# Performance work log

Measured on AMD Instinct MI355X. Metric: run time of the kernel, lower is better.

The kernel has to match this reference:

```python
import jax, jax.numpy as jnp
import numpy as np

D_H, HEAD, LAYER_IDX = 1024, 16, 11
D_ATTN = D_H // HEAD
BZ, LEN = 2, 2048


def setup_inputs() -> dict:
    key = jax.random.key(0)
    ks = jax.random.split(key, 8)
    s = 1.0 / np.sqrt(D_H)
    v = jax.random.normal(ks[0], (BZ, LEN, D_H), jnp.float32)
    k = jax.random.normal(ks[1], (BZ, LEN, D_H), jnp.float32)
    q = jax.random.normal(ks[2], (BZ, LEN, D_H), jnp.float32)
    # causal mask: 1.0 where attention is blocked (j > i)
    causal = jnp.triu(jnp.ones((LEN, LEN), jnp.float32), k=1)
    mask = jnp.broadcast_to(causal[None, None], (BZ, 1, LEN, LEN))
    Wv = jax.random.normal(ks[3], (D_H, D_H), jnp.float32) * s
    Wk = jax.random.normal(ks[4], (D_H, D_H), jnp.float32) * s
    Wq = jax.random.normal(ks[5], (D_H, D_H), jnp.float32) * s
    Wo = jax.random.normal(ks[6], (D_H, D_H), jnp.float32) * s
    bo = jnp.zeros((D_H,), jnp.float32)
    return {"v": v, "k": k, "q": q, "mask": mask,
            "Wv": Wv, "Wk": Wk, "Wq": Wq, "Wo": Wo, "bo": bo}


def _split_head(x):
    # (bz, len, d_h) -> (bz, head, len, d_attn)
    bz, L, _ = x.shape
    return x.reshape(bz, L, HEAD, D_ATTN).transpose(0, 2, 1, 3)


def reference(v, k, q, mask, Wv, Wk, Wq, Wo, bo):
    bz, len_q, _ = q.shape
    vh = _split_head(v @ Wv)  # (bz, head, len_k, d_attn)
    kh = _split_head(k @ Wk)
    qh = _split_head(q @ Wq)
    scale = 1.0 / jnp.sqrt(jnp.asarray(D_ATTN, jnp.float32))
    weight = jnp.einsum("bhqd,bhkd->bhqk", qh, kh) * scale
    weight = weight + mask * (-1e9)
    weight = weight / jnp.asarray(LAYER_IDX + 1, jnp.float32)
    attn = jax.nn.softmax(weight, axis=-1)  # dropout omitted (inference)
    out = jnp.einsum("bhqk,bhkd->bhqd", attn, vh)
    out = out.transpose(0, 2, 1, 3).reshape(bz, len_q, D_H)
    return out @ Wo + bo
```

## Files before the change

### kernel.cpp

```cpp
#include <hip/hip_runtime.h>
#include <hip/hip_fp16.h>

typedef _Float16 f16;
typedef _Float16 f16x4 __attribute__((ext_vector_type(4)));
typedef _Float16 f16x8 __attribute__((ext_vector_type(8)));
typedef float f32x4 __attribute__((ext_vector_type(4)));
typedef float f32x16 __attribute__((ext_vector_type(16)));

#define D_H   1024
#define LEN   2048
#define BZ    2
#define NHEAD 16
#define DA    64
#define MTOK  (BZ * LEN)
#define KDIM  1024
#define ATT_SCALE (0.125f / 12.0f)

__device__ __forceinline__ void load_lds16(const f16* g, f16* l) {
  __builtin_amdgcn_global_load_lds((const __attribute__((address_space(1))) void*)g,
                                   (__attribute__((address_space(3))) void*)l,
                                   16, 0, 0);
}

#define FENCE() __asm__ volatile("" ::: "memory")

__device__ __forceinline__ unsigned pk2(float a, float b) {
  union { f16 h; unsigned short u; } ca, cb;
  ca.h = (f16)a; cb.h = (f16)b;
  return (unsigned)ca.u | ((unsigned)cb.u << 16);
}

__global__ __launch_bounds__(256)
void k_prep(const float* __restrict__ W0, const float* __restrict__ W1,
            const float* __restrict__ W2, const float* __restrict__ W3,
            const float* __restrict__ xq, const float* __restrict__ xk,
            const float* __restrict__ xv,
            f16* __restrict__ T0, f16* __restrict__ T1,
            f16* __restrict__ T2, f16* __restrict__ T3,
            f16* __restrict__ q16, f16* __restrict__ k16,
            f16* __restrict__ v16) {
  const int z = blockIdx.z;
  const int tid = threadIdx.x;
  if (z < 4) {
    const float* W = (z == 0) ? W0 : (z == 1) ? W1 : (z == 2) ? W2 : W3;
    f16* Wt = (z == 0) ? T0 : (z == 1) ? T1 : (z == 2) ? T2 : T3;
    __shared__ float tile[64][68];
    const int r0 = blockIdx.y * 64, c0 = blockIdx.x * 64;
    {
      const int row = tid >> 2, cq = (tid & 3) * 16;
      const float* src = W + (size_t)(r0 + row) * D_H + c0 + cq;
      float4 v0 = *(const float4*)(src + 0);
      float4 v1 = *(const float4*)(src + 4);
      float4 v2 = *(const float4*)(src + 8);
      float4 v3 = *(const float4*)(src + 12);
      *(float4*)&tile[row][cq + 0]  = v0;
      *(float4*)&tile[row][cq + 4]  = v1;
      *(float4*)&tile[row][cq + 8]  = v2;
      *(float4*)&tile[row][cq + 12] = v3;
    }
    __syncthreads();
    {
      const int c = tid >> 2, rq = (tid & 3) * 16;
      f16 ov[16];
#pragma unroll
      for (int j = 0; j < 16; ++j) ov[j] = (f16)tile[rq + j][c];
      f16* dst = Wt + (size_t)(c0 + c) * D_H + r0 + rq;
      *(f16x8*)(dst + 0) = *(f16x8*)&ov[0];
      *(f16x8*)(dst + 8) = *(f16x8*)&ov[8];
    }
  } else {
    const float* in = (z == 4) ? xq : (z == 5) ? xk : xv;
    f16* out = (z == 4) ? q16 : (z == 5) ? k16 : v16;
    const size_t blk = ((size_t)(blockIdx.y * 16 + blockIdx.x)) * 16384;
#pragma unroll
    for (int s = 0; s < 16; ++s) {
      size_t off = blk + (size_t)(s * 256 + tid) * 4;
      float4 x = *(const float4*)(in + off);
      f16x4 o; o[0] = (f16)x.x; o[1] = (f16)x.y; o[2] = (f16)x.z; o[3] = (f16)x.w;
      *(f16x4*)(out + off) = o;
    }
  }
}

#define BM2 256
#define BN2 256
#define BKT 64
#define NKT (KDIM / BKT)

__global__ __launch_bounds__(512, 2)
void k_gemm3(const f16* __restrict__ A0, const f16* __restrict__ A1,
             const f16* __restrict__ A2, const f16* __restrict__ W0,
             const f16* __restrict__ W1, const f16* __restrict__ W2,
             f16* __restrict__ O0, f16* __restrict__ O1, f16* __restrict__ O2) {
  __shared__ __align__(16) f16 smem3[65536];
  f16* As = smem3;
  f16* Bs = smem3 + 32768;
  const int lin = blockIdx.x + 16 * blockIdx.y + 64 * blockIdx.z;
  const int w = (lin & 7) * 24 + (lin >> 3);
  const int z = w >> 6;
  const int rem = w & 63;
  const int m0 = (rem >> 2) * BM2, n0 = (rem & 3) * BN2;
  const f16* A = (z == 0) ? A0 : (z == 1) ? A1 : A2;
  const f16* Bt = (z == 0) ? W0 : (z == 1) ? W1 : W2;
  f16* Out = (z == 0) ? O0 : (z == 1) ? O1 : O2;
  const int tid = threadIdx.x;
  const int wave = tid >> 6, lane = tid & 63;
  const int lc = lane & 15, quad = lane >> 4;
  const int wr = wave >> 2, wc = wave & 3;
  const f16* Ab = A + (size_t)m0 * KDIM;
  const f16* Bb = Bt + (size_t)n0 * KDIM;

  f32x4 acc[8][4] = {};

#define STAGE_HALF(g, ldsbase, kt, h)                                         \
  {                                                                           \
    _Pragma("unroll")                                                         \
    for (int r = 0; r < 2; ++r) {                                             \
      int idx = tid + r * 512;                                                \
      int row = (h) * 128 + (idx >> 3);                                       \
      int gch = (idx & 7) ^ (row & 7);                                        \
      load_lds16((g) + (size_t)row * KDIM + (kt) * BKT + gch * 8,             \
                 (ldsbase) + (h) * 8192 + idx * 8);                           \
    }                                                                         \
  }

#define READ_A(mh, kc)                                                        \
  _Pragma("unroll")                                                           \
  for (int i = 0; i < 4; ++i) {                                               \
    int row = wr * 128 + ((mh) * 4 + i) * 16 + lc;                            \
    int pc = ((kc) * 4 + quad) ^ (row & 7);                                   \
    af[i] = *(const f16x8*)&Ad[row * 64 + pc * 8];                            \
  }
#define READ_B(kc)                                                            \
  _Pragma("unroll")                                                           \
  for (int n = 0; n < 4; ++n) {                                               \
    int row = wc * 64 + n * 16 + lc;                                          \
    int pc = ((kc) * 4 + quad) ^ (row & 7);                                   \
    bf[n] = *(const f16x8*)&Bd[row * 64 + pc * 8];                            \
  }
#define MFMA_Q(mh)                                                            \
  FENCE(); __builtin_amdgcn_s_barrier();                                      \
  __builtin_amdgcn_s_setprio(1);                                              \
  _Pragma("unroll")                                                           \
  for (int i = 0; i < 4; ++i)                                                 \
    _Pragma("unroll")                                                         \
    for (int n = 0; n < 4; ++n)                                               \
      acc[(mh) * 4 + i][n] = __builtin_amdgcn_mfma_f32_16x16x32_f16(          \
          af[i], bf[n], acc[(mh) * 4 + i][n], 0, 0, 0);                       \
  __builtin_amdgcn_s_setprio(0);                                              \
  __asm__ volatile("s_waitcnt lgkmcnt(0)" ::: "memory");                      \
  FENCE(); __builtin_amdgcn_s_barrier(); FENCE();

  STAGE_HALF(Ab, As, 0, 0);
  STAGE_HALF(Ab, As, 0, 1);
  STAGE_HALF(Bb, Bs, 0, 0);
  STAGE_HALF(Bb, Bs, 0, 1);
  STAGE_HALF(Ab, As + 16384, 1, 0);
  __asm__ volatile("s_waitcnt vmcnt(2)" ::: "memory");
  __builtin_amdgcn_s_barrier();
  FENCE();

  for (int t = 0; t < NKT; ++t) {
    const f16* Ad = As + (t & 1) * 16384;
    const f16* Bd = Bs + (t & 1) * 16384;
    f16* AdW = As + (t & 1) * 16384;
    f16* Adn = As + ((t + 1) & 1) * 16384;
    f16* Bdn = Bs + ((t + 1) & 1) * 16384;
    const bool pf = (t + 1 < NKT);
    f16x8 af[4], bf[4];

    READ_A(0, 0); READ_B(0);
    if (pf) STAGE_HALF(Ab, Adn, t + 1, 1);
    MFMA_Q(0);

    READ_A(1, 0);
    if (pf) STAGE_HALF(Bb, Bdn, t + 1, 0);
    MFMA_Q(1);

    READ_A(0, 1); READ_B(1);
    if (pf) STAGE_HALF(Bb, Bdn, t + 1, 1);
    MFMA_Q(0);

    READ_A(1, 1);
    FENCE(); __builtin_amdgcn_s_barrier();
    if (t + 2 < NKT) STAGE_HALF(Ab, AdW, t + 2, 0);
    __builtin_amdgcn_s_setprio(1);
#pragma unroll
    for (int i = 0; i < 4; ++i)
#pragma unroll
      for (int n = 0; n < 4; ++n)
        acc[4 + i][n] = __builtin_amdgcn_mfma_f32_16x16x32_f16(
            af[i], bf[n], acc[4 + i][n], 0, 0, 0);
    __builtin_amdgcn_s_setprio(0);
    if (t + 2 < NKT) {
      __asm__ volatile("s_waitcnt vmcnt(2)" ::: "memory");
    } else if (pf) {
      __asm__ volatile("s_waitcnt vmcnt(0)" ::: "memory");
    }
    __asm__ volatile("s_waitcnt lgkmcnt(0)" ::: "memory");
    FENCE(); __builtin_amdgcn_s_barrier(); FENCE();
  }

  if (z <= 1) {
    f16* slice = smem3 + wave * 8192;
#pragma unroll
    for (int mi = 0; mi < 8; ++mi)
#pragma unroll
      for (int ni = 0; ni < 4; ++ni)
#pragma unroll
        for (int rr = 0; rr < 4; ++rr) {
          int tl = mi * 16 + quad * 4 + rr;
          int d = ni * 16 + lc;
          slice[tl * 64 + (((d >> 3) ^ (tl & 7)) << 3) + (d & 7)] =
              (f16)acc[mi][ni][rr];
        }
    __asm__ volatile("s_waitcnt lgkmcnt(0)" ::: "memory");
    const int h = (n0 >> 6) + wc;
    const int tokbase = m0 + wr * 128;
    const int b = tokbase >> 11, ib = tokbase & 2047;
#pragma unroll
    for (int s = 0; s < 16; ++s) {
      int u = lane + s * 64;
      int tl = u >> 3, ch = u & 7;
      f16x8 vv = *(const f16x8*)&slice[tl * 64 + ((ch ^ (tl & 7)) << 3)];
      *(f16x8*)(Out + ((size_t)((b << 4) + h) * LEN + ib + tl) * DA + ch * 8) = vv;
    }
  } else {
    f16* Ct = smem3;
#pragma unroll
    for (int e = 0; e < 2; ++e) {
      __syncthreads();
      if (wr == e) {
#pragma unroll
        for (int mi = 0; mi < 8; ++mi)
#pragma unroll
          for (int ni = 0; ni < 4; ++ni)
#pragma unroll
            for (int rr = 0; rr < 4; ++rr) {
              int tl = mi * 16 + quad * 4 + rr;
              int dl = wc * 64 + ni * 16 + lc;
              Ct[dl * 136 + tl] = (f16)acc[mi][ni][rr];
            }
      }
      __syncthreads();
      const int tokbase = m0 + e * 128;
      const int b = tokbase >> 11, j0 = tokbase & 2047;
#pragma unroll
      for (int s = 0; s < 8; ++s) {
        int u = tid + s * 512;
        int dl = u >> 4, ch = u & 15;
        f16x8 vv = *(const f16x8*)&Ct[dl * 136 + ch * 8];
        *(f16x8*)(Out + ((size_t)(b * 1024 + n0 + dl)) * LEN + j0 + ch * 8) = vv;
      }
    }
  }
}

#define OM 64
#define ON 128
#define BK 64
#define ONIT (KDIM / BK)
__global__ __launch_bounds__(256)
void k_gemm_out(const f16* __restrict__ A, const f16* __restrict__ Bt,
                float* __restrict__ Out, const float* __restrict__ bias) {
  __shared__ __align__(16) char smem[2 * (OM + ON) * BK * 2];
  f16* As = (f16*)smem;
  f16* Bs = As + 2 * OM * BK;
  const int m0 = blockIdx.x * OM, n0 = blockIdx.y * ON;
  const int tid = threadIdx.x;
  const int wave = tid >> 6, lane = tid & 63;
  const int lc = lane & 15, quad = lane >> 4;
  const int wm = (wave >> 1) * 32, wn = (wave & 1) * 64;
  const int swz = lc & 7;
  const f16* Abase = A + (size_t)m0 * KDIM;
  const f16* Bbase = Bt + (size_t)n0 * KDIM;

  f32x4 acc[2][4] = {};

#define STAGE_OUT(t)                                                          \
  {                                                                           \
    int k0s = (t) * BK;                                                       \
    f16* Ad = As + ((t) & 1) * (OM * BK);                                     \
    f16* Bd = Bs + ((t) & 1) * (ON * BK);                                     \
    _Pragma("unroll")                                                         \
    for (int r = 0; r < 2; ++r) {                                             \
      int idx = tid + r * 256;                                                \
      int row = idx >> 3, ch = idx & 7;                                       \
      int gch = ch ^ (row & 7);                                               \
      load_lds16(Abase + (size_t)row * KDIM + k0s + gch * 8, &Ad[idx * 8]);   \
    }                                                                         \
    _Pragma("unroll")                                                         \
    for (int r = 0; r < 4; ++r) {                                             \
      int idx = tid + r * 256;                                                \
      int row = idx >> 3, ch = idx & 7;                                       \
      int gch = ch ^ (row & 7);                                               \
      load_lds16(Bbase + (size_t)row * KDIM + k0s + gch * 8, &Bd[idx * 8]);   \
    }                                                                         \
  }

  STAGE_OUT(0);
  for (int t = 0; t < ONIT; ++t) {
    __syncthreads();
    if (t + 1 < ONIT) STAGE_OUT(t + 1);
    const f16* Ad = As + (t & 1) * (OM * BK);
    const f16* Bd = Bs + (t & 1) * (ON * BK);
    __builtin_amdgcn_s_setprio(1);
#pragma unroll
    for (int kc = 0; kc < 2; ++kc) {
      f16x8 af[2], bf[4];
#pragma unroll
      for (int mi = 0; mi < 2; ++mi)
        af[mi] = *(const f16x8*)&Ad[(wm + mi * 16 + lc) * 64 +
                                    (((kc * 4 + quad) ^ swz) * 8)];
#pragma unroll
      for (int ni = 0; ni < 4; ++ni)
        bf[ni] = *(const f16x8*)&Bd[(wn + ni * 16 + lc) * 64 +
                                    (((kc * 4 + quad) ^ swz) * 8)];
#pragma unroll
      for (int mi = 0; mi < 2; ++mi)
#pragma unroll
        for (int ni = 0; ni < 4; ++ni)
          acc[mi][ni] = __builtin_amdgcn_mfma_f32_16x16x32_f16(
              af[mi], bf[ni], acc[mi][ni], 0, 0, 0);
    }
    __builtin_amdgcn_s_setprio(0);
  }

  float* Ct = (float*)smem;
#pragma unroll
  for (int hf = 0; hf < 2; ++hf) {
    __syncthreads();
    if ((wave & 1) == hf) {
#pragma unroll
      for (int mi = 0; mi < 2; ++mi)
#pragma unroll
        for (int ni = 0; ni < 4; ++ni)
#pragma unroll
          for (int r = 0; r < 4; ++r) {
            int tok = wm + mi * 16 + quad * 4 + r;
            int d = ni * 16 + lc;
            Ct[tok * 68 + d] = acc[mi][ni][r];
          }
    }
    __syncthreads();
#pragma unroll
    for (int it = 0; it < 4; ++it) {
      int u = tid + it * 256;
      int tok = u >> 4, ch = u & 15;
      int gm = m0 + tok;
      int gc = n0 + hf * 64 + ch * 4;
      float4 bv = *(const float4*)(bias + gc);
      float4 cv = *(const float4*)&Ct[tok * 68 + ch * 4];
      float4 ov;
      ov.x = cv.x + bv.x; ov.y = cv.y + bv.y;
      ov.z = cv.z + bv.z; ov.w = cv.w + bv.w;
      *(float4*)(Out + (size_t)gm * D_H + gc) = ov;
    }
  }
}

__global__ __launch_bounds__(256, 2)
void k_attn(const f16* __restrict__ Qh, const f16* __restrict__ Kh,
            const f16* __restrict__ Vt, f16* __restrict__ O16) {
  const int tid = threadIdx.x;
  const int wid = blockIdx.x * 4 + (tid >> 6);
  const int lane = tid & 63;
  const int cq = lane & 31, half = lane >> 5;
  const int jb = (wid < 1024) ? (63 - (wid >> 5)) : ((wid - 1024) >> 5);
  const int bh = wid & 31;
  const int b = bh >> 4, h = bh & 15;
  const f16* Qb = Qh + (size_t)bh * LEN * DA;
  const f16* Kb = Kh + (size_t)bh * LEN * DA;
  const f16* Vb = Vt + (size_t)bh * DA * LEN;
  const f16 qs = (f16)(ATT_SCALE * 1.44269504088896340736f);

  f16x8 qf[4];
#pragma unroll
  for (int d = 0; d < 4; ++d) {
    qf[d] = *(const f16x8*)(Qb + (size_t)(jb * 32 + cq) * DA + d * 16 + half * 8);
#pragma unroll
    for (int j = 0; j < 8; ++j) qf[d][j] = qf[d][j] * qs;
  }

  f32x16 acc0 = {}, acc1 = {};
  float lsum = 0.f;

#define AT_LOAD(tt, KF, VF)                                                   \
  {                                                                           \
    const f16* kp = Kb + (size_t)((tt) * 32 + cq) * DA + half * 8;            \
    KF[0] = *(const f16x8*)(kp);                                              \
    KF[1] = *(const f16x8*)(kp + 16);                                         \
    KF[2] = *(const f16x8*)(kp + 32);                                         \
    KF[3] = *(const f16x8*)(kp + 48);                                         \
    const f16* vp0 = Vb + (size_t)cq * LEN + (tt) * 32 + half * 8;            \
    const f16* vp1 = Vb + (size_t)(32 + cq) * LEN + (tt) * 32 + half * 8;     \
    VF[0] = *(const f16x8*)(vp0);                                             \
    VF[1] = *(const f16x8*)(vp1);                                             \
    VF[2] = *(const f16x8*)(vp0 + 16);                                        \
    VF[3] = *(const f16x8*)(vp1 + 16);                                        \
  }

#define AT_COMPUTE(tt, KF, VF)                                                \
  {                                                                           \
    f32x16 st = {};                                                           \
    st = __builtin_amdgcn_mfma_f32_32x32x16_f16(KF[0], qf[0], st, 0, 0, 0);   \
    st = __builtin_amdgcn_mfma_f32_32x32x16_f16(KF[1], qf[1], st, 0, 0, 0);   \
    st = __builtin_amdgcn_mfma_f32_32x32x16_f16(KF[2], qf[2], st, 0, 0, 0);   \
    st = __builtin_amdgcn_mfma_f32_32x32x16_f16(KF[3], qf[3], st, 0, 0, 0);   \
    float ev[16];                                                             \
    if ((tt) == jb) {                                                         \
      _Pragma("unroll")                                                       \
      for (int r = 0; r < 16; ++r) {                                          \
        int kl = (r & 3) + 8 * (r >> 2) + 4 * half;                           \
        float e = exp2f(st[r]);                                               \
        ev[r] = (kl > cq) ? 0.f : e;                                          \
      }                                                                       \
    } else {                                                                  \
      _Pragma("unroll")                                                       \
      for (int r = 0; r < 16; ++r) ev[r] = exp2f(st[r]);                      \
    }                                                                         \
    lsum += (((ev[0] + ev[1]) + (ev[2] + ev[3])) +                            \
             ((ev[4] + ev[5]) + (ev[6] + ev[7]))) +                           \
            (((ev[8] + ev[9]) + (ev[10] + ev[11])) +                          \
             ((ev[12] + ev[13]) + (ev[14] + ev[15])));                        \
    unsigned w0 = pk2(ev[0], ev[1]),  w1 = pk2(ev[2], ev[3]);                 \
    unsigned w2 = pk2(ev[4], ev[5]),  w3 = pk2(ev[6], ev[7]);                 \
    unsigned w4 = pk2(ev[8], ev[9]),  w5 = pk2(ev[10], ev[11]);               \
    unsigned w6 = pk2(ev[12], ev[13]), w7 = pk2(ev[14], ev[15]);              \
    unsigned p0 = __shfl_xor((int)w0, 32, 64), p1 = __shfl_xor((int)w1, 32, 64);\
    unsigned p2 = __shfl_xor((int)w2, 32, 64), p3 = __shfl_xor((int)w3, 32, 64);\
    unsigned p4 = __shfl_xor((int)w4, 32, 64), p5 = __shfl_xor((int)w5, 32, 64);\
    unsigned p6 = __shfl_xor((int)w6, 32, 64), p7 = __shfl_xor((int)w7, 32, 64);\
    union { unsigned u[4]; f16x8 v; } A0, A1;                                 \
    A0.u[0] = half ? p2 : w0;  A0.u[1] = half ? p3 : w1;                      \
    A0.u[2] = half ? w2 : p0;  A0.u[3] = half ? w3 : p1;                      \
    A1.u[0] = half ? p6 : w4;  A1.u[1] = half ? p7 : w5;                      \
    A1.u[2] = half ? w6 : p4;  A1.u[3] = half ? w7 : p5;                      \
    acc0 = __builtin_amdgcn_mfma_f32_32x32x16_f16(A0.v, VF[0], acc0, 0, 0, 0);\
    acc1 = __builtin_amdgcn_mfma_f32_32x32x16_f16(A0.v, VF[1], acc1, 0, 0, 0);\
    acc0 = __builtin_amdgcn_mfma_f32_32x32x16_f16(A1.v, VF[2], acc0, 0, 0, 0);\
    acc1 = __builtin_amdgcn_mfma_f32_32x32x16_f16(A1.v, VF[3], acc1, 0, 0, 0);\
  }

  f16x8 kfA[4], vfA[4], kfB[4], vfB[4];
  const int niter = jb + 1;
  AT_LOAD(0, kfA, vfA);
  int t = 0;
  for (; t + 1 < niter; t += 2) {
    AT_LOAD(t + 1, kfB, vfB);
    AT_COMPUTE(t, kfA, vfA);
    if (t + 2 < niter) AT_LOAD(t + 2, kfA, vfA);
    AT_COMPUTE(t + 1, kfB, vfB);
  }
  if (t < niter) AT_COMPUTE(t, kfA, vfA);

  lsum += __shfl_xor(lsum, 32, 64);
  const size_t obase = ((size_t)b * LEN + jb * 32) * D_H + h * DA;
#pragma unroll
  for (int r = 0; r < 16; ++r) {
    int rq = (r & 3) + 8 * (r >> 2) + 4 * half;
    float ls = __shfl(lsum, rq, 64);
    float inv = 1.0f / ls;
    O16[obase + (size_t)rq * D_H + cq] = (f16)(acc0[r] * inv);
    O16[obase + (size_t)rq * D_H + 32 + cq] = (f16)(acc1[r] * inv);
  }
}

extern "C" void kernel_launch(void* const* d_in, const int* in_sizes, int n_in,
                              void* d_out, int out_size, void* d_ws, size_t ws_size,
                              hipStream_t stream) {
  const float* v_f = (const float*)d_in[0];
  const float* k_f = (const float*)d_in[1];
  const float* q_f = (const float*)d_in[2];
  const float* Wv = (const float*)d_in[4];
  const float* Wk = (const float*)d_in[5];
  const float* Wq = (const float*)d_in[6];
  const float* Wo = (const float*)d_in[7];
  const float* bo = (const float*)d_in[8];
  float* out = (float*)d_out;

  const size_t SZ_X = (size_t)MTOK * D_H;
  const size_t SZ_W = (size_t)D_H * D_H;
  f16* ws = (f16*)d_ws;
  f16* q16 = ws;
  f16* k16 = ws + SZ_X;
  f16* v16 = ws + 2 * SZ_X;
  f16* Qh  = ws + 3 * SZ_X;
  f16* Kh  = ws + 4 * SZ_X;
  f16* Vt  = ws + 5 * SZ_X;
  f16* Wqt = ws + 6 * SZ_X;
  f16* Wkt = Wqt + SZ_W;
  f16* Wvt = Wqt + 2 * SZ_W;
  f16* Wot = Wqt + 3 * SZ_W;
  f16* O16 = q16;

  k_prep<<<dim3(16, 16, 7), 256, 0, stream>>>(
      Wq, Wk, Wv, Wo, q_f, k_f, v_f, Wqt, Wkt, Wvt, Wot, q16, k16, v16);

  k_gemm3<<<dim3(MTOK / BM2, D_H / BN2, 3), 512, 0, stream>>>(
      q16, k16, v16, Wqt, Wkt, Wvt, Qh, Kh, Vt);

  k_attn<<<dim3(512), 256, 0, stream>>>(Qh, Kh, Vt, O16);

  k_gemm_out<<<dim3(MTOK / OM, D_H / ON), 256, 0, stream>>>(O16, Wot, out, bo);
}
```

Measured before the change: 244.0 us.

## Split attention key range across wave pairs and combine partials via LDS

Each query tile is now processed by two waves that each cover half of the causal key tiles. The second wave writes its partial accumulators and row sums to shared memory, and the first wave adds them and writes the normalized output. The grid doubles and launch bounds rise to 4 blocks per CU. The aim is to shorten the critical path of long causal rows and raise occupancy, at the cost of a block-wide sync, an LDS reduction and register pressure under the tighter bound.

Result: slower. 336.5 us (+37.9%).

```diff
diff --git a/kernel.cpp b/kernel.cpp
--- a/kernel.cpp
+++ b/kernel.cpp
@@ -359,20 +359,27 @@
   }
 }
 
-__global__ __launch_bounds__(256, 2)
+__global__ __launch_bounds__(256, 4)
 void k_attn(const f16* __restrict__ Qh, const f16* __restrict__ Kh,
             const f16* __restrict__ Vt, f16* __restrict__ O16) {
+  __shared__ float comb[2][64][33];
   const int tid = threadIdx.x;
-  const int wid = blockIdx.x * 4 + (tid >> 6);
-  const int lane = tid & 63;
+  const int wave = tid >> 6, lane = tid & 63;
   const int cq = lane & 31, half = lane >> 5;
-  const int jb = (wid < 1024) ? (63 - (wid >> 5)) : ((wid - 1024) >> 5);
-  const int bh = wid & 31;
+  const int pairId = wave >> 1, ks = wave & 1;
+  const int bh = blockIdx.x & 31;
+  const int p = blockIdx.x >> 5;
+  const int jb = pairId ? p : 63 - p;
   const int b = bh >> 4, h = bh & 15;
   const f16* Qb = Qh + (size_t)bh * LEN * DA;
   const f16* Kb = Kh + (size_t)bh * LEN * DA;
   const f16* Vb = Vt + (size_t)bh * DA * LEN;
   const f16 qs = (f16)(ATT_SCALE * 1.44269504088896340736f);
+
+  const int nT = jb + 1;
+  const int nA = (nT + 1) >> 1;
+  const int t0 = ks ? nA : 0;
+  const int cnt = ks ? (nT - nA) : nA;
 
   f16x8 qf[4];
 #pragma unroll
@@ -442,27 +449,46 @@
     acc1 = __builtin_amdgcn_mfma_f32_32x32x16_f16(A1.v, VF[3], acc1, 0, 0, 0);\
   }
 
-  f16x8 kfA[4], vfA[4], kfB[4], vfB[4];
-  const int niter = jb + 1;
-  AT_LOAD(0, kfA, vfA);
-  int t = 0;
-  for (; t + 1 < niter; t += 2) {
-    AT_LOAD(t + 1, kfB, vfB);
-    AT_COMPUTE(t, kfA, vfA);
-    if (t + 2 < niter) AT_LOAD(t + 2, kfA, vfA);
-    AT_COMPUTE(t + 1, kfB, vfB);
-  }
-  if (t < niter) AT_COMPUTE(t, kfA, vfA);
-
-  lsum += __shfl_xor(lsum, 32, 64);
-  const size_t obase = ((size_t)b * LEN + jb * 32) * D_H + h * DA;
-#pragma unroll
-  for (int r = 0; r < 16; ++r) {
-    int rq = (r & 3) + 8 * (r >> 2) + 4 * half;
-    float ls = __shfl(lsum, rq, 64);
-    float inv = 1.0f / ls;
-    O16[obase + (size_t)rq * D_H + cq] = (f16)(acc0[r] * inv);
-    O16[obase + (size_t)rq * D_H + 32 + cq] = (f16)(acc1[r] * inv);
+  if (cnt > 0) {
+    f16x8 kfA[4], vfA[4], kfB[4], vfB[4];
+    const int tend = t0 + cnt;
+    AT_LOAD(t0, kfA, vfA);
+    int t = t0;
+    for (; t + 1 < tend; t += 2) {
+      AT_LOAD(t + 1, kfB, vfB);
+      AT_COMPUTE(t, kfA, vfA);
+      if (t + 2 < tend) AT_LOAD(t + 2, kfA, vfA);
+      AT_COMPUTE(t + 1, kfB, vfB);
+    }
+    if (t < tend) AT_COMPUTE(t, kfA, vfA);
+  }
+
+  if (ks == 1) {
+#pragma unroll
+    for (int r = 0; r < 16; ++r) {
+      comb[pairId][lane][r] = acc0[r];
+      comb[pairId][lane][16 + r] = acc1[r];
+    }
+    comb[pairId][lane][32] = lsum;
+  }
+  __syncthreads();
+  if (ks == 0) {
+#pragma unroll
+    for (int r = 0; r < 16; ++r) {
+      acc0[r] += comb[pairId][lane][r];
+      acc1[r] += comb[pairId][lane][16 + r];
+    }
+    lsum += comb[pairId][lane][32];
+    lsum += __shfl_xor(lsum, 32, 64);
+    const size_t obase = ((size_t)b * LEN + jb * 32) * D_H + h * DA;
+#pragma unroll
+    for (int r = 0; r < 16; ++r) {
+      int rq = (r & 3) + 8 * (r >> 2) + 4 * half;
+      float ls = __shfl(lsum, rq, 64);
+      float inv = 1.0f / ls;
+      O16[obase + (size_t)rq * D_H + cq] = (f16)(acc0[r] * inv);
+      O16[obase + (size_t)rq * D_H + 32 + cq] = (f16)(acc1[r] * inv);
+    }
   }
 }
 
@@ -500,7 +526,7 @@
   k_gemm3<<<dim3(MTOK / BM2, D_H / BN2, 3), 512, 0, stream>>>(
       q16, k16, v16, Wqt, Wkt, Wvt, Qh, Kh, Vt);
 
-  k_attn<<<dim3(512), 256, 0, stream>>>(Qh, Kh, Vt, O16);
+  k_attn<<<dim3(1024), 256, 0, stream>>>(Qh, Kh, Vt, O16);
 
   k_gemm_out<<<dim3(MTOK / OM, D_H / ON), 256, 0, stream>>>(O16, Wot, out, bo);
 }
```
